# Optimization experiments

Measured on AMD Instinct MI355X. Metric: run time of the kernel, lower is better.

The kernel has to match this reference:

```python
import jax, jax.numpy as jnp
import numpy as np

DECAY = 0.97
TEMP = 0.7
EPS = 1e-6
NORM_EPS = 1e-12  # torch F.normalize default eps


def _l2norm(x, axis=-1):
    n = jnp.linalg.norm(x, axis=axis, keepdims=True)
    return x / jnp.maximum(n, NORM_EPS)


def setup_inputs() -> dict:
    key = jax.random.key(0)
    k1, k2, k3 = jax.random.split(key, 3)
    pair_embed = jax.random.normal(k1, (8, 2048, 1024), dtype=jnp.float32)
    patterns = _l2norm(jax.random.normal(k2, (4096, 1024), dtype=jnp.float32))
    usage = jax.random.uniform(k3, (4096,), dtype=jnp.float32)
    return {"pair_embed": pair_embed, "patterns": patterns, "usage": usage}


def reference(pair_embed, patterns, usage):
    G, D = patterns.shape
    flat = pair_embed.reshape(-1, D)                      # [N, D]
    queries = _l2norm(flat)
    pat_n = _l2norm(patterns)
    logits = queries @ pat_n.T                             # [N, G]
    homeostasis = jnp.log(jnp.clip(usage, EPS))
    weights = jax.nn.softmax((logits - homeostasis[None, :]) / TEMP, axis=-1)

    # Hebbian EMA update (mirrors update(); no_grad in original)
    flat_assign = weights                                  # [N, G]
    weights_sum = flat_assign.sum(axis=0)                  # [G]
    valid = weights_sum > 0
    usage_new = usage * DECAY
    usage_new = jnp.where(valid, usage_new + (1.0 - DECAY) * weights_sum, usage_new)
    updates = flat_assign.T @ flat                         # [G, D]
    updates = updates / (weights_sum[:, None] + EPS)
    blended = _l2norm(patterns * DECAY + (1.0 - DECAY) * updates)
    patterns_new = jnp.where(valid[:, None], blended, patterns)

    out_weights = weights.reshape(*pair_embed.shape[:-1], G)
    return out_weights, patterns_new, usage_new
```

## Files before the change

### kernel.cpp

```cpp
#include <hip/hip_runtime.h>
#include <stdint.h>
#include <math.h>


#define DECAY 0.97f
#define OMD 0.03f
#define INV_TEMP (1.0f / 0.7f)
#define EPS 1e-6f
#define NORM_EPS 1e-12f

constexpr int NROWS = 16384;
constexpr int DK = 1024;
constexpr int GP = 4096;

typedef unsigned short u16;
typedef __bf16 bf16x8 __attribute__((ext_vector_type(8)));
typedef float f32x4 __attribute__((ext_vector_type(4)));

__device__ inline u16 f2bf(float x) {
    union { float f; uint32_t u; } c; c.f = x;
    uint32_t r = c.u + 0x7fffu + ((c.u >> 16) & 1u);
    return (u16)(r >> 16);
}

__device__ inline void gl_lds16(const u16* g, u16* l) {
    __builtin_amdgcn_global_load_lds(
        (const __attribute__((address_space(1))) void*)g,
        (__attribute__((address_space(3))) void*)l, 16, 0, 0);
}

__global__ __launch_bounds__(256) void norm_rows_kernel(
        const float* __restrict__ in, u16* __restrict__ outn) {
    __shared__ float sred[4];
    const int row = blockIdx.x;
    const int t = threadIdx.x;
    const float4 v = ((const float4*)(in + (size_t)row * DK))[t];
    float ss = v.x * v.x + v.y * v.y + v.z * v.z + v.w * v.w;
#pragma unroll
    for (int o = 32; o > 0; o >>= 1) ss += __shfl_xor(ss, o);
    if ((t & 63) == 0) sred[t >> 6] = ss;
    __syncthreads();
    const float tot = sred[0] + sred[1] + sred[2] + sred[3];
    const float rs = 1.0f / fmaxf(sqrtf(tot), NORM_EPS);
    ushort4 o4;
    o4.x = f2bf(v.x * rs); o4.y = f2bf(v.y * rs);
    o4.z = f2bf(v.z * rs); o4.w = f2bf(v.w * rs);
    ((ushort4*)(outn + (size_t)row * DK))[t] = o4;
}

__global__ __launch_bounds__(256) void prep_scalars_kernel(
        const float* __restrict__ usage, float* __restrict__ hscaled,
        float* __restrict__ wsum) {
    const int g = blockIdx.x * 256 + threadIdx.x;
    if (g < GP) {
        hscaled[g] = logf(fmaxf(usage[g], EPS)) * INV_TEMP;
        wsum[g] = 0.0f;
    }
}

__global__ __launch_bounds__(256) void zero_kernel(float4* __restrict__ p) {
    p[(size_t)blockIdx.x * 256 + threadIdx.x] = (float4){0.f, 0.f, 0.f, 0.f};
}

__global__ __launch_bounds__(256) void transpose_f32_bf16_kernel(
        const float* __restrict__ in, u16* __restrict__ out, int R, int C) {
    __shared__ float tile[64][260];
    const int r0 = blockIdx.x * 64;
    const int c0 = blockIdx.y * 256;
    const int t = threadIdx.x;
    const int fr = t & 63;
    const int rr = t >> 6;
#pragma unroll
    for (int j = 0; j < 16; ++j) {
        const int r = rr + 4 * j;
        const float4 v = *(const float4*)(in + (size_t)(r0 + r) * C + c0 + fr * 4);
        *(float4*)&tile[r][fr * 4] = v;
    }
    __syncthreads();
    __align__(16) u16 tmp[64];
#pragma unroll
    for (int r = 0; r < 64; ++r) tmp[r] = f2bf(tile[r][t]);
    u16* op = out + (size_t)(c0 + t) * R + r0;
#pragma unroll
    for (int i = 0; i < 8; ++i) ((uint4*)op)[i] = ((const uint4*)tmp)[i];
}

template <int KSTEPS, int KLD>
__device__ inline void gemm_bt_tile(const u16* __restrict__ A,
                                    const u16* __restrict__ B,
                                    int m0, int n0, int k0,
                                    u16* As, u16* Bs, f32x4 acc[4][4]) {
    const int t = threadIdx.x;
    const int lane = t & 63;
    const int wave = t >> 6;
    const int wm = (wave >> 1) * 64;
    const int wn = (wave & 1) * 64;
    const int fr = lane & 15;
    const int q8 = lane >> 4;

    const int srow = 32 * wave + (lane >> 3);
    const int soct = (lane & 7) ^ ((lane >> 3) & 7);
    const size_t a_base = (size_t)(m0 + srow) * KLD + k0 + soct * 8;
    const size_t b_base = (size_t)(n0 + srow) * KLD + k0 + soct * 8;

#pragma unroll 1
    for (int kt = 0; kt < KSTEPS; kt += 64) {
        __syncthreads();
#pragma unroll
        for (int i = 0; i < 4; ++i) {
            gl_lds16(A + a_base + (size_t)(8 * i) * KLD + kt,
                     As + (32 * wave + 8 * i) * 64);
            gl_lds16(B + b_base + (size_t)(8 * i) * KLD + kt,
                     Bs + (32 * wave + 8 * i) * 64);
        }
        __syncthreads();
#pragma unroll
        for (int ks8 = 0; ks8 < 8; ks8 += 4) {
            bf16x8 af[4], bfr[4];
#pragma unroll
            for (int f = 0; f < 4; ++f) {
                const int ra = wm + f * 16 + fr;
                af[f]  = *(const bf16x8*)(As + ra * 64 + (((ks8 + q8) ^ (ra & 7)) * 8));
                const int rb = wn + f * 16 + fr;
                bfr[f] = *(const bf16x8*)(Bs + rb * 64 + (((ks8 + q8) ^ (rb & 7)) * 8));
            }
#pragma unroll
            for (int fm = 0; fm < 4; ++fm)
#pragma unroll
                for (int fn = 0; fn < 4; ++fn)
                    acc[fm][fn] = __builtin_amdgcn_mfma_f32_16x16x32_bf16(
                        af[fm], bfr[fn], acc[fm][fn], 0, 0, 0);
        }
    }
}

__global__ __launch_bounds__(256) void gemm1_kernel(
        const u16* __restrict__ Q, const u16* __restrict__ P,
        const float* __restrict__ hs, float* __restrict__ Wout) {
    __shared__ u16 As[128 * 64];
    __shared__ u16 Bs[128 * 64];
    const int bid = blockIdx.x;
    const int m0 = (bid >> 5) * 128;
    const int n0 = (bid & 31) * 128;
    f32x4 acc[4][4];
#pragma unroll
    for (int a = 0; a < 4; ++a)
#pragma unroll
        for (int b = 0; b < 4; ++b) acc[a][b] = (f32x4){0.f, 0.f, 0.f, 0.f};
    gemm_bt_tile<DK, DK>(Q, P, m0, n0, 0, As, Bs, acc);

    const int lane = threadIdx.x & 63;
    const int wave = threadIdx.x >> 6;
    const int wm = (wave >> 1) * 64, wn = (wave & 1) * 64;
    const int cq = lane & 15, rq = (lane >> 4) * 4;
#pragma unroll
    for (int fn = 0; fn < 4; ++fn) {
        const int g = n0 + wn + fn * 16 + cq;
        const float h = hs[g];
#pragma unroll
        for (int fm = 0; fm < 4; ++fm) {
            const int mb = m0 + wm + fm * 16 + rq;
#pragma unroll
            for (int r = 0; r < 4; ++r)
                Wout[(size_t)(mb + r) * GP + g] = acc[fm][fn][r] * INV_TEMP - h;
        }
    }
}

__global__ __launch_bounds__(256) void gemm2_kernel(
        const u16* __restrict__ WT, const u16* __restrict__ FT,
        float* __restrict__ Upart) {
    __shared__ u16 As[128 * 64];
    __shared__ u16 Bs[128 * 64];
    const int bid = blockIdx.x;
    const int k0 = (bid & 7) * 2048;
    const int n0 = ((bid >> 3) & 7) * 128;
    const int m0 = (bid >> 6) * 128;
    f32x4 acc[4][4];
#pragma unroll
    for (int a = 0; a < 4; ++a)
#pragma unroll
        for (int b = 0; b < 4; ++b) acc[a][b] = (f32x4){0.f, 0.f, 0.f, 0.f};
    gemm_bt_tile<2048, NROWS>(WT, FT, m0, n0, k0, As, Bs, acc);

    const int lane = threadIdx.x & 63;
    const int wave = threadIdx.x >> 6;
    const int wm = (wave >> 1) * 64, wn = (wave & 1) * 64;
    const int cq = lane & 15, rq = (lane >> 4) * 4;
#pragma unroll
    for (int fn = 0; fn < 4; ++fn) {
        const int d = n0 + wn + fn * 16 + cq;
#pragma unroll
        for (int fm = 0; fm < 4; ++fm) {
            const int gb = m0 + wm + fm * 16 + rq;
#pragma unroll
            for (int r = 0; r < 4; ++r)
                atomicAdd(&Upart[(size_t)(gb + r) * DK + d], acc[fm][fn][r]);
        }
    }
}

__global__ __launch_bounds__(256) void softmax_kernel(
        float* __restrict__ W, float* __restrict__ wsum) {
    __shared__ float sred[4];
    const int t = threadIdx.x;
    float cs[4][4];
#pragma unroll
    for (int j = 0; j < 4; ++j)
#pragma unroll
        for (int i = 0; i < 4; ++i) cs[j][i] = 0.f;

    for (int r = 0; r < 32; ++r) {
        float4* Wr = (float4*)(W + (size_t)(blockIdx.x * 32 + r) * GP);
        float4 v[4];
        float m = -INFINITY;
#pragma unroll
        for (int j = 0; j < 4; ++j) {
            v[j] = Wr[t + j * 256];
            m = fmaxf(m, fmaxf(fmaxf(v[j].x, v[j].y), fmaxf(v[j].z, v[j].w)));
        }
#pragma unroll
        for (int o = 32; o > 0; o >>= 1) m = fmaxf(m, __shfl_xor(m, o));
        if ((t & 63) == 0) sred[t >> 6] = m;
        __syncthreads();
        m = fmaxf(fmaxf(sred[0], sred[1]), fmaxf(sred[2], sred[3]));
        __syncthreads();
        float s = 0.f;
#pragma unroll
        for (int j = 0; j < 4; ++j) {
            v[j].x = __expf(v[j].x - m); v[j].y = __expf(v[j].y - m);
            v[j].z = __expf(v[j].z - m); v[j].w = __expf(v[j].w - m);
            s += v[j].x + v[j].y + v[j].z + v[j].w;
        }
#pragma unroll
        for (int o = 32; o > 0; o >>= 1) s += __shfl_xor(s, o);
        if ((t & 63) == 0) sred[t >> 6] = s;
        __syncthreads();
        s = sred[0] + sred[1] + sred[2] + sred[3];
        __syncthreads();
        const float inv = 1.0f / s;
#pragma unroll
        for (int j = 0; j < 4; ++j) {
            v[j].x *= inv; v[j].y *= inv; v[j].z *= inv; v[j].w *= inv;
            Wr[t + j * 256] = v[j];
            cs[j][0] += v[j].x; cs[j][1] += v[j].y;
            cs[j][2] += v[j].z; cs[j][3] += v[j].w;
        }
    }
#pragma unroll
    for (int j = 0; j < 4; ++j)
#pragma unroll
        for (int i = 0; i < 4; ++i)
            atomicAdd(&wsum[4 * t + 1024 * j + i], cs[j][i]);
}

__global__ __launch_bounds__(256) void usage_kernel(
        const float* __restrict__ usage, const float* __restrict__ wsum,
        float* __restrict__ Uout, float* __restrict__ invw) {
    const int g = blockIdx.x * 256 + threadIdx.x;
    if (g < GP) {
        const float s = wsum[g];
        Uout[g] = usage[g] * DECAY + (s > 0.f ? OMD * s : 0.f);
        invw[g] = 1.0f / (s + EPS);
    }
}

__global__ __launch_bounds__(256) void finalize_patterns_kernel(
        const float* __restrict__ patterns, const float* __restrict__ wsum,
        const float* __restrict__ invw, const float* __restrict__ Upart,
        float* __restrict__ Pout) {
    __shared__ float sred[4];
    const int g = blockIdx.x;
    const int t = threadIdx.x;
    const float iw = invw[g] * OMD;
    const float4 u4 = ((const float4*)(Upart + (size_t)g * DK))[t];
    const float4 p4 = ((const float4*)(patterns + (size_t)g * DK))[t];
    float4 b;
    b.x = DECAY * p4.x + iw * u4.x;
    b.y = DECAY * p4.y + iw * u4.y;
    b.z = DECAY * p4.z + iw * u4.z;
    b.w = DECAY * p4.w + iw * u4.w;
    float ss = b.x * b.x + b.y * b.y + b.z * b.z + b.w * b.w;
#pragma unroll
    for (int o = 32; o > 0; o >>= 1) ss += __shfl_xor(ss, o);
    if ((t & 63) == 0) sred[t >> 6] = ss;
    __syncthreads();
    const float tot = sred[0] + sred[1] + sred[2] + sred[3];
    const float rs = 1.0f / fmaxf(sqrtf(tot), NORM_EPS);
    float4 o4;
    if (wsum[g] > 0.f) {
        o4.x = b.x * rs; o4.y = b.y * rs; o4.z = b.z * rs; o4.w = b.w * rs;
    } else {
        o4 = p4;
    }
    ((float4*)(Pout + (size_t)g * DK))[t] = o4;
}

extern "C" void kernel_launch(void* const* d_in, const int* in_sizes, int n_in,
                              void* d_out, int out_size, void* d_ws, size_t ws_size,
                              hipStream_t stream) {
    const float* pair_embed = (const float*)d_in[0];
    const float* patterns   = (const float*)d_in[1];
    const float* usage      = (const float*)d_in[2];

    float* out_w = (float*)d_out;
    float* out_p = out_w + (size_t)NROWS * GP;
    float* out_u = out_p + (size_t)GP * DK;

    char* ws = (char*)d_ws;
    u16* q_bf   = (u16*)(ws);
    float* Upart = (float*)(ws);
    u16* pat_bf = (u16*)(ws + 33554432);
    u16* fT     = (u16*)(ws + 41943040);
    u16* wT     = (u16*)(ws + 75497472);
    float* hs   = (float*)(ws + 209715200);
    float* wsum = (float*)(ws + 209715200 + 16384);
    float* invw = (float*)(ws + 209715200 + 32768);

    prep_scalars_kernel<<<16, 256, 0, stream>>>(usage, hs, wsum);
    norm_rows_kernel<<<NROWS, 256, 0, stream>>>(pair_embed, q_bf);
    norm_rows_kernel<<<GP, 256, 0, stream>>>(patterns, pat_bf);
    {
        dim3 g(NROWS / 64, DK / 256);
        transpose_f32_bf16_kernel<<<g, 256, 0, stream>>>(pair_embed, fT, NROWS, DK);
    }
    gemm1_kernel<<<(NROWS / 128) * (GP / 128), 256, 0, stream>>>(q_bf, pat_bf, hs, out_w);
    softmax_kernel<<<NROWS / 32, 256, 0, stream>>>(out_w, wsum);
    usage_kernel<<<16, 256, 0, stream>>>(usage, wsum, out_u, invw);
    zero_kernel<<<(GP * DK / 4) / 256, 256, 0, stream>>>((float4*)Upart);
    {
        dim3 g(NROWS / 64, GP / 256);
        transpose_f32_bf16_kernel<<<g, 256, 0, stream>>>(out_w, wT, NROWS, GP);
    }
    gemm2_kernel<<<8 * (GP / 128) * (DK / 128), 256, 0, stream>>>(wT, fT, Upart);
    finalize_patterns_kernel<<<GP, 256, 0, stream>>>(patterns, wsum, invw, Upart, out_p);
}
```

Before: 971.3 us.

## Fuse softmax exp into GEMM epilogue and normalization into transpose pass

```diff
diff --git a/kernel.cpp b/kernel.cpp
--- a/kernel.cpp
+++ b/kernel.cpp
@@ -50,12 +50,18 @@
 
 __global__ __launch_bounds__(256) void prep_scalars_kernel(
         const float* __restrict__ usage, float* __restrict__ hscaled,
-        float* __restrict__ wsum) {
-    const int g = blockIdx.x * 256 + threadIdx.x;
-    if (g < GP) {
-        hscaled[g] = logf(fmaxf(usage[g], EPS)) * INV_TEMP;
-        wsum[g] = 0.0f;
-    }
+        float* __restrict__ wsum, float* __restrict__ rowsum) {
+    const int i = blockIdx.x * 256 + threadIdx.x;
+    if (i < GP) {
+        hscaled[i] = logf(fmaxf(usage[i], EPS)) * INV_TEMP;
+        wsum[i] = 0.0f;
+    }
+    rowsum[i] = 0.0f;
+}
+
+__global__ __launch_bounds__(256) void rowinv_kernel(float* __restrict__ rowsum) {
+    const int i = blockIdx.x * 256 + threadIdx.x;
+    rowsum[i] = 1.0f / rowsum[i];
 }
 
 __global__ __launch_bounds__(256) void zero_kernel(float4* __restrict__ p) {
@@ -83,6 +89,42 @@
     u16* op = out + (size_t)(c0 + t) * R + r0;
 #pragma unroll
     for (int i = 0; i < 8; ++i) ((uint4*)op)[i] = ((const uint4*)tmp)[i];
+}
+
+__global__ __launch_bounds__(256) void scale_transpose_kernel(
+        float* __restrict__ W, const float* __restrict__ invs,
+        u16* __restrict__ wT, float* __restrict__ wsum) {
+    __shared__ float tile[64][260];
+    __shared__ float sinv[64];
+    const int r0 = blockIdx.x * 64;
+    const int c0 = blockIdx.y * 256;
+    const int t = threadIdx.x;
+    if (t < 64) sinv[t] = invs[r0 + t];
+    __syncthreads();
+    const int fr = t & 63;
+    const int rr = t >> 6;
+#pragma unroll
+    for (int j = 0; j < 16; ++j) {
+        const int r = rr + 4 * j;
+        float4 v = *(const float4*)(W + (size_t)(r0 + r) * GP + c0 + fr * 4);
+        const float s = sinv[r];
+        v.x *= s; v.y *= s; v.z *= s; v.w *= s;
+        *(float4*)(W + (size_t)(r0 + r) * GP + c0 + fr * 4) = v;
+        *(float4*)&tile[r][fr * 4] = v;
+    }
+    __syncthreads();
+    __align__(16) u16 tmp[64];
+    float csum = 0.f;
+#pragma unroll
+    for (int r = 0; r < 64; ++r) {
+        const float x = tile[r][t];
+        csum += x;
+        tmp[r] = f2bf(x);
+    }
+    u16* op = wT + (size_t)(c0 + t) * NROWS + r0;
+#pragma unroll
+    for (int i = 0; i < 8; ++i) ((uint4*)op)[i] = ((const uint4*)tmp)[i];
+    atomicAdd(&wsum[c0 + t], csum);
 }
 
 template <int KSTEPS, int KLD>
@@ -136,10 +178,12 @@
 
 __global__ __launch_bounds__(256) void gemm1_kernel(
         const u16* __restrict__ Q, const u16* __restrict__ P,
-        const float* __restrict__ hs, float* __restrict__ Wout) {
+        const float* __restrict__ hs, float* __restrict__ Wout,
+        float* __restrict__ rowsum) {
     __shared__ u16 As[128 * 64];
     __shared__ u16 Bs[128 * 64];
-    const int bid = blockIdx.x;
+    const int bid0 = blockIdx.x;
+    const int bid = (bid0 & 7) * 512 + (bid0 >> 3);
     const int m0 = (bid >> 5) * 128;
     const int n0 = (bid & 31) * 128;
     f32x4 acc[4][4];
@@ -153,16 +197,25 @@
     const int wave = threadIdx.x >> 6;
     const int wm = (wave >> 1) * 64, wn = (wave & 1) * 64;
     const int cq = lane & 15, rq = (lane >> 4) * 4;
-#pragma unroll
-    for (int fn = 0; fn < 4; ++fn) {
-        const int g = n0 + wn + fn * 16 + cq;
-        const float h = hs[g];
-#pragma unroll
-        for (int fm = 0; fm < 4; ++fm) {
-            const int mb = m0 + wm + fm * 16 + rq;
-#pragma unroll
-            for (int r = 0; r < 4; ++r)
-                Wout[(size_t)(mb + r) * GP + g] = acc[fm][fn][r] * INV_TEMP - h;
+    float hval[4];
+#pragma unroll
+    for (int fn = 0; fn < 4; ++fn) hval[fn] = hs[n0 + wn + fn * 16 + cq];
+#pragma unroll
+    for (int fm = 0; fm < 4; ++fm) {
+        const int mb = m0 + wm + fm * 16 + rq;
+#pragma unroll
+        for (int r = 0; r < 4; ++r) {
+            float rs = 0.f;
+#pragma unroll
+            for (int fn = 0; fn < 4; ++fn) {
+                const int g = n0 + wn + fn * 16 + cq;
+                const float e = __expf(acc[fm][fn][r] * INV_TEMP - hval[fn]);
+                Wout[(size_t)(mb + r) * GP + g] = e;
+                rs += e;
+            }
+#pragma unroll
+            for (int o = 1; o < 16; o <<= 1) rs += __shfl_xor(rs, o);
+            if (cq == 0) atomicAdd(&rowsum[mb + r], rs);
         }
     }
 }
@@ -200,60 +253,6 @@
     }
 }
 
-__global__ __launch_bounds__(256) void softmax_kernel(
-        float* __restrict__ W, float* __restrict__ wsum) {
-    __shared__ float sred[4];
-    const int t = threadIdx.x;
-    float cs[4][4];
-#pragma unroll
-    for (int j = 0; j < 4; ++j)
-#pragma unroll
-        for (int i = 0; i < 4; ++i) cs[j][i] = 0.f;
-
-    for (int r = 0; r < 32; ++r) {
-        float4* Wr = (float4*)(W + (size_t)(blockIdx.x * 32 + r) * GP);
-        float4 v[4];
-        float m = -INFINITY;
-#pragma unroll
-        for (int j = 0; j < 4; ++j) {
-            v[j] = Wr[t + j * 256];
-            m = fmaxf(m, fmaxf(fmaxf(v[j].x, v[j].y), fmaxf(v[j].z, v[j].w)));
-        }
-#pragma unroll
-        for (int o = 32; o > 0; o >>= 1) m = fmaxf(m, __shfl_xor(m, o));
-        if ((t & 63) == 0) sred[t >> 6] = m;
-        __syncthreads();
-        m = fmaxf(fmaxf(sred[0], sred[1]), fmaxf(sred[2], sred[3]));
-        __syncthreads();
-        float s = 0.f;
-#pragma unroll
-        for (int j = 0; j < 4; ++j) {
-            v[j].x = __expf(v[j].x - m); v[j].y = __expf(v[j].y - m);
-            v[j].z = __expf(v[j].z - m); v[j].w = __expf(v[j].w - m);
-            s += v[j].x + v[j].y + v[j].z + v[j].w;
-        }
-#pragma unroll
-        for (int o = 32; o > 0; o >>= 1) s += __shfl_xor(s, o);
-        if ((t & 63) == 0) sred[t >> 6] = s;
-        __syncthreads();
-        s = sred[0] + sred[1] + sred[2] + sred[3];
-        __syncthreads();
-        const float inv = 1.0f / s;
-#pragma unroll
-        for (int j = 0; j < 4; ++j) {
-            v[j].x *= inv; v[j].y *= inv; v[j].z *= inv; v[j].w *= inv;
-            Wr[t + j * 256] = v[j];
-            cs[j][0] += v[j].x; cs[j][1] += v[j].y;
-            cs[j][2] += v[j].z; cs[j][3] += v[j].w;
-        }
-    }
-#pragma unroll
-    for (int j = 0; j < 4; ++j)
-#pragma unroll
-        for (int i = 0; i < 4; ++i)
-            atomicAdd(&wsum[4 * t + 1024 * j + i], cs[j][i]);
-}
-
 __global__ __launch_bounds__(256) void usage_kernel(
         const float* __restrict__ usage, const float* __restrict__ wsum,
         float* __restrict__ Uout, float* __restrict__ invw) {
@@ -316,22 +315,23 @@
     float* hs   = (float*)(ws + 209715200);
     float* wsum = (float*)(ws + 209715200 + 16384);
     float* invw = (float*)(ws + 209715200 + 32768);
-
-    prep_scalars_kernel<<<16, 256, 0, stream>>>(usage, hs, wsum);
+    float* rsum = (float*)(ws + 209715200 + 49152);
+
+    prep_scalars_kernel<<<64, 256, 0, stream>>>(usage, hs, wsum, rsum);
     norm_rows_kernel<<<NROWS, 256, 0, stream>>>(pair_embed, q_bf);
     norm_rows_kernel<<<GP, 256, 0, stream>>>(patterns, pat_bf);
     {
         dim3 g(NROWS / 64, DK / 256);
         transpose_f32_bf16_kernel<<<g, 256, 0, stream>>>(pair_embed, fT, NROWS, DK);
     }
-    gemm1_kernel<<<(NROWS / 128) * (GP / 128), 256, 0, stream>>>(q_bf, pat_bf, hs, out_w);
-    softmax_kernel<<<NROWS / 32, 256, 0, stream>>>(out_w, wsum);
+    gemm1_kernel<<<(NROWS / 128) * (GP / 128), 256, 0, stream>>>(q_bf, pat_bf, hs, out_w, rsum);
+    rowinv_kernel<<<64, 256, 0, stream>>>(rsum);
+    {
+        dim3 g(NROWS / 64, GP / 256);
+        scale_transpose_kernel<<<g, 256, 0, stream>>>(out_w, rsum, wT, wsum);
+    }
     usage_kernel<<<16, 256, 0, stream>>>(usage, wsum, out_u, invw);
     zero_kernel<<<(GP * DK / 4) / 256, 256, 0, stream>>>((float4*)Upart);
-    {
-        dim3 g(NROWS / 64, GP / 256);
-        transpose_f32_bf16_kernel<<<g, 256, 0, stream>>>(out_w, wT, NROWS, GP);
-    }
     gemm2_kernel<<<8 * (GP / 128) * (DK / 128), 256, 0, stream>>>(wT, fT, Upart);
     finalize_patterns_kernel<<<GP, 256, 0, stream>>>(patterns, wsum, invw, Upart, out_p);
 }
```

After: 925.9 us. 1.05x faster.
